# Optimization experiments

Hardware: AMD Instinct MI355X
Metric: run time of the kernel (lower is better)

## Reference

```python
import jax, jax.numpy as jnp
import numpy as np

N = 4_194_304          # number of rays
DAMPING = 0.5          # LM(0.5)
MAX_DELTA = 1000.0     # clamp on LM step
N_ITER = 30            # no_grad warmup iterations
XMIN, XMAX, TAU = -1.0, 1.0, 1.0


def _surface_F(pts, c):
    # implicit parabolic rod: F(p) = x - c*(y^2 + z^2); pts: [N,3]
    return pts[..., 0] - c * (pts[..., 1] ** 2 + pts[..., 2] ** 2)


def _lm_delta(P, V, t, c):
    # Levenberg-Marquardt step for f(t) = F(P + t*V):
    # delta = f * f' / (f'^2 + damping), clamped to [-max_delta, max_delta]
    pts = P + t[:, None] * V                     # [N,3]
    f = _surface_F(pts, c)                       # [N]
    # f'(t) = gradF(pts) . V, gradF = (1, -2c*y, -2c*z)
    fp = V[:, 0] - 2.0 * c * (pts[:, 1] * V[:, 1] + pts[:, 2] * V[:, 2])
    delta = f * fp / (fp * fp + DAMPING)
    return jnp.clip(delta, -MAX_DELTA, MAX_DELTA)


def setup_inputs() -> dict:
    key = jax.random.key(0)
    k1, k2 = jax.random.split(key, 2)
    P = jax.random.normal(k1, (N, 3), jnp.float32) * 2.0
    V = jax.random.normal(k2, (N, 3), jnp.float32)
    V = V / jnp.linalg.norm(V, axis=-1, keepdims=True)
    a, b = 0.3, -0.2
    Rz = jnp.array([[np.cos(a), -np.sin(a), 0.0],
                    [np.sin(a),  np.cos(a), 0.0],
                    [0.0,        0.0,       1.0]], jnp.float32)
    Ry = jnp.array([[np.cos(b), 0.0, np.sin(b)],
                    [0.0,       1.0, 0.0],
                    [-np.sin(b), 0.0, np.cos(b)]], jnp.float32)
    R = Rz @ Ry                                  # rigid rotation [3,3]
    T = jnp.array([0.1, -0.2, 0.05], jnp.float32)
    c = jnp.float32(0.05)
    loss_in = jnp.float32(0.0)
    return {"P": P, "V": V, "R": R, "T": T, "c": c, "loss_in": loss_in}


def reference(P, V, R, T, c, loss_in):
    n = P.shape[0]
    # transform.inverse_points / inverse_vectors: R^T (p - T), R^T v
    P_local = (P - T) @ R                        # [N,3]
    V_local = V @ R                              # [N,3]

    # 30 no-grad LM iterations (torch.no_grad -> stop_gradient on inputs)
    Pl = jax.lax.stop_gradient(P_local)
    Vl = jax.lax.stop_gradient(V_local)
    cs = jax.lax.stop_gradient(c)

    def body(i, t):
        return t - _lm_delta(Pl, Vl, t, cs)

    t0 = jax.lax.fori_loop(0, N_ITER, body, jnp.zeros((n,), jnp.float32))

    # final differentiable LM step
    t = t0 - _lm_delta(P_local, V_local, t0, c)

    points_local = P_local + t[:, None] * V_local
    scale = jnp.mean(jnp.abs(jnp.array([XMIN, XMAX, TAU], jnp.float32)))
    F = _surface_F(points_local, c) / scale
    loss = loss_in + jnp.sum(F ** 2) / n
    return loss
```

## Files before the change

kernel.cpp:

```cpp
#include <hip/hip_runtime.h>


#define LM_ITERS 31
constexpr float DAMPING = 0.5f;

__global__ __launch_bounds__(256) void rod_kernel(
    const float* __restrict__ P, const float* __restrict__ V,
    const float* __restrict__ Rm, const float* __restrict__ Tv,
    const float* __restrict__ c_ptr, double* __restrict__ ws, int n)
{
    const float c  = c_ptr[0];
    const float r00 = Rm[0], r01 = Rm[1], r02 = Rm[2];
    const float r10 = Rm[3], r11 = Rm[4], r12 = Rm[5];
    const float r20 = Rm[6], r21 = Rm[7], r22 = Rm[8];
    const float t0 = Tv[0], t1 = Tv[1], t2 = Tv[2];

    const int tid      = blockIdx.x * blockDim.x + threadIdx.x;
    const int nthreads = gridDim.x * blockDim.x;

    const float4* P4 = (const float4*)P;
    const float4* V4 = (const float4*)V;

    double acc = 0.0;

    float nA[4], f[4], fp[4];
    auto setup4 = [&](const float4& qa, const float4& qb, const float4& qc,
                      const float4& ua, const float4& ub, const float4& uc) {
        const float px[4] = {qa.x, qa.w, qb.z, qc.y};
        const float py[4] = {qa.y, qb.x, qb.w, qc.z};
        const float pz[4] = {qa.z, qb.y, qc.x, qc.w};
        const float wx[4] = {ua.x, ua.w, ub.z, uc.y};
        const float wy[4] = {ua.y, ub.x, ub.w, uc.z};
        const float wz[4] = {ua.z, ub.y, uc.x, uc.w};
        #pragma unroll
        for (int r = 0; r < 4; ++r) {
            const float qx = px[r] - t0, qy = py[r] - t1, qz = pz[r] - t2;
            const float plx = qx * r00 + qy * r10 + qz * r20;
            const float ply = qx * r01 + qy * r11 + qz * r21;
            const float plz = qx * r02 + qy * r12 + qz * r22;
            const float vlx = wx[r] * r00 + wy[r] * r10 + wz[r] * r20;
            const float vly = wx[r] * r01 + wy[r] * r11 + wz[r] * r21;
            const float vlz = wx[r] * r02 + wy[r] * r12 + wz[r] * r22;
            nA[r] = c * (vly * vly + vlz * vlz);
            f[r]  = plx - c * (ply * ply + plz * plz);
            fp[r] = vlx - 2.0f * c * (ply * vly + plz * vlz);
        }
    };

    auto iterate = [&]() {
        #pragma unroll 1
        for (int it = 0; it < LM_ITERS; ++it) {
            #pragma unroll
            for (int r = 0; r < 4; ++r) {
                const float den = fmaf(fp[r], fp[r], DAMPING);
                const float rcp = __builtin_amdgcn_rcpf(den);
                const float d   = (f[r] * fp[r]) * rcp;
                const float tmp = fmaf(nA[r], d, fp[r]);
                f[r]  = fmaf(-d, tmp, f[r]);
                fp[r] = fmaf(nA[r], d, tmp);
            }
        }
    };

    auto accum = [&](int g) {
        #pragma unroll
        for (int r = 0; r < 4; ++r)
            if (4 * g + r < n) acc += (double)f[r] * (double)f[r];
    };

    const int g0 = tid;
    const int g1 = tid + nthreads;
    const int g2 = tid + 2 * nthreads;
    const int g3 = tid + 3 * nthreads;

    float4 a0{}, b0{}, c0{}, u0{}, v0{}, w0{};
    if (4 * g0 < n) {
        a0 = P4[g0 * 3 + 0]; b0 = P4[g0 * 3 + 1]; c0 = P4[g0 * 3 + 2];
        u0 = V4[g0 * 3 + 0]; v0 = V4[g0 * 3 + 1]; w0 = V4[g0 * 3 + 2];
    }
    setup4(a0, b0, c0, u0, v0, w0);

    float4 a1{}, b1{}, c1{}, u1{}, v1{}, w1{};
    if (4 * g1 < n) {
        a1 = P4[g1 * 3 + 0]; b1 = P4[g1 * 3 + 1]; c1 = P4[g1 * 3 + 2];
        u1 = V4[g1 * 3 + 0]; v1 = V4[g1 * 3 + 1]; w1 = V4[g1 * 3 + 2];
    }
    iterate();
    accum(g0);

    setup4(a1, b1, c1, u1, v1, w1);
    float4 a2{}, b2{}, c2{}, u2{}, v2{}, w2{};
    if (4 * g2 < n) {
        a2 = P4[g2 * 3 + 0]; b2 = P4[g2 * 3 + 1]; c2 = P4[g2 * 3 + 2];
        u2 = V4[g2 * 3 + 0]; v2 = V4[g2 * 3 + 1]; w2 = V4[g2 * 3 + 2];
    }
    iterate();
    accum(g1);

    setup4(a2, b2, c2, u2, v2, w2);
    float4 a3{}, b3{}, c3{}, u3{}, v3{}, w3{};
    if (4 * g3 < n) {
        a3 = P4[g3 * 3 + 0]; b3 = P4[g3 * 3 + 1]; c3 = P4[g3 * 3 + 2];
        u3 = V4[g3 * 3 + 0]; v3 = V4[g3 * 3 + 1]; w3 = V4[g3 * 3 + 2];
    }
    iterate();
    accum(g2);

    setup4(a3, b3, c3, u3, v3, w3);
    iterate();
    accum(g3);

    for (int off = 32; off > 0; off >>= 1)
        acc += __shfl_down(acc, off, 64);
    __shared__ double sacc[4];
    const int lane = threadIdx.x & 63, wave = threadIdx.x >> 6;
    if (lane == 0) sacc[wave] = acc;
    __syncthreads();
    if (threadIdx.x == 0) {
        atomicAdd(ws, sacc[0] + sacc[1] + sacc[2] + sacc[3]);
    }
}

__global__ void rod_finalize(const double* __restrict__ ws,
                             const float* __restrict__ loss_in,
                             float* __restrict__ out, double inv_n)
{
    out[0] = (float)(ws[0] * inv_n + (double)loss_in[0]);
}

extern "C" void kernel_launch(void* const* d_in, const int* in_sizes, int n_in,
                              void* d_out, int out_size, void* d_ws, size_t ws_size,
                              hipStream_t stream) {
    const float* P       = (const float*)d_in[0];
    const float* V       = (const float*)d_in[1];
    const float* R       = (const float*)d_in[2];
    const float* T       = (const float*)d_in[3];
    const float* c       = (const float*)d_in[4];
    const float* loss_in = (const float*)d_in[5];

    const int n = in_sizes[0] / 3;

    hipMemsetAsync(d_ws, 0, sizeof(double), stream);

    const int threads = (n + 15) / 16;
    const int block   = 256;
    const int grid    = (threads + block - 1) / block;
    rod_kernel<<<grid, block, 0, stream>>>(P, V, R, T, c, (double*)d_ws, n);
    rod_finalize<<<1, 1, 0, stream>>>((const double*)d_ws, loss_in,
                                      (float*)d_out, 1.0 / (double)n);
}
```

Baseline: 135.6 us.

## Stage ray loads through LDS with global_load_lds, one group of rays per thread

Replaces the four-group-per-thread grid-stride scheme, which prefetched the next group during the LM loop, with one group of four rays per thread and four times as many threads. Each wave loads its contiguous P and V chunk into LDS with global_load_lds direct-to-LDS copies, so the global loads are fully coalesced, then reads the interleaved xyz back per lane. The cost is losing the software overlap of loads with compute and quadrupling the block count and atomics, relying on occupancy instead. A scalar fallback path handles partial tail waves.

```diff
diff --git a/kernel.cpp b/kernel.cpp
--- a/kernel.cpp
+++ b/kernel.cpp
@@ -1,8 +1,12 @@
 #include <hip/hip_runtime.h>
+#include <stdint.h>
 
 
 #define LM_ITERS 31
 constexpr float DAMPING = 0.5f;
+
+typedef __attribute__((address_space(3))) uint32_t lds_u32_t;
+typedef __attribute__((address_space(1))) const uint32_t glob_u32_t;
 
 __global__ __launch_bounds__(256) void rod_kernel(
     const float* __restrict__ P, const float* __restrict__ V,
@@ -15,105 +19,100 @@
     const float r20 = Rm[6], r21 = Rm[7], r22 = Rm[8];
     const float t0 = Tv[0], t1 = Tv[1], t2 = Tv[2];
 
-    const int tid      = blockIdx.x * blockDim.x + threadIdx.x;
-    const int nthreads = gridDim.x * blockDim.x;
+    __shared__ float4 sh[4][192];
 
-    const float4* P4 = (const float4*)P;
-    const float4* V4 = (const float4*)V;
+    const int lane = threadIdx.x & 63;
+    const int wave = threadIdx.x >> 6;
+    const int wave_ray_base = blockIdx.x * 1024 + wave * 256;
+    const int base_ray      = wave_ray_base + 4 * lane;
+
+    float px[4], py[4], pz[4], wx[4], wy[4], wz[4];
+
+    if (wave_ray_base + 256 <= n) {
+        const size_t wq = (size_t)(wave_ray_base >> 2) * 3;
+        const char* gP = (const char*)P + wq * 16;
+        const char* gV = (const char*)V + wq * 16;
+
+        #pragma unroll
+        for (int j = 0; j < 3; ++j) {
+            __builtin_amdgcn_global_load_lds(
+                (glob_u32_t*)(gP + (size_t)(j * 64 + lane) * 16),
+                (lds_u32_t*)&sh[wave][j * 64 + lane], 16, 0, 0);
+        }
+        asm volatile("s_waitcnt vmcnt(0)" ::: "memory");
+        const float4 pa = sh[wave][lane * 3 + 0];
+        const float4 pb = sh[wave][lane * 3 + 1];
+        const float4 pc = sh[wave][lane * 3 + 2];
+        asm volatile("s_waitcnt lgkmcnt(0)" ::: "memory");
+
+        #pragma unroll
+        for (int j = 0; j < 3; ++j) {
+            __builtin_amdgcn_global_load_lds(
+                (glob_u32_t*)(gV + (size_t)(j * 64 + lane) * 16),
+                (lds_u32_t*)&sh[wave][j * 64 + lane], 16, 0, 0);
+        }
+        asm volatile("s_waitcnt vmcnt(0)" ::: "memory");
+        const float4 va = sh[wave][lane * 3 + 0];
+        const float4 vb = sh[wave][lane * 3 + 1];
+        const float4 vc = sh[wave][lane * 3 + 2];
+        asm volatile("s_waitcnt lgkmcnt(0)" ::: "memory");
+
+        px[0] = pa.x; px[1] = pa.w; px[2] = pb.z; px[3] = pc.y;
+        py[0] = pa.y; py[1] = pb.x; py[2] = pb.w; py[3] = pc.z;
+        pz[0] = pa.z; pz[1] = pb.y; pz[2] = pc.x; pz[3] = pc.w;
+        wx[0] = va.x; wx[1] = va.w; wx[2] = vb.z; wx[3] = vc.y;
+        wy[0] = va.y; wy[1] = vb.x; wy[2] = vb.w; wy[3] = vc.z;
+        wz[0] = va.z; wz[1] = vb.y; wz[2] = vc.x; wz[3] = vc.w;
+    } else {
+        #pragma unroll
+        for (int r = 0; r < 4; ++r) {
+            const int ray = base_ray + r;
+            if (ray < n) {
+                px[r] = P[3 * ray + 0]; py[r] = P[3 * ray + 1]; pz[r] = P[3 * ray + 2];
+                wx[r] = V[3 * ray + 0]; wy[r] = V[3 * ray + 1]; wz[r] = V[3 * ray + 2];
+            } else {
+                px[r] = py[r] = pz[r] = 0.0f;
+                wx[r] = wy[r] = wz[r] = 0.0f;
+            }
+        }
+    }
+
+    float nA[4], f[4], fp[4];
+    #pragma unroll
+    for (int r = 0; r < 4; ++r) {
+        const float qx = px[r] - t0, qy = py[r] - t1, qz = pz[r] - t2;
+        const float plx = qx * r00 + qy * r10 + qz * r20;
+        const float ply = qx * r01 + qy * r11 + qz * r21;
+        const float plz = qx * r02 + qy * r12 + qz * r22;
+        const float vlx = wx[r] * r00 + wy[r] * r10 + wz[r] * r20;
+        const float vly = wx[r] * r01 + wy[r] * r11 + wz[r] * r21;
+        const float vlz = wx[r] * r02 + wy[r] * r12 + wz[r] * r22;
+        nA[r] = c * (vly * vly + vlz * vlz);
+        f[r]  = plx - c * (ply * ply + plz * plz);
+        fp[r] = vlx - 2.0f * c * (ply * vly + plz * vlz);
+    }
+
+    #pragma unroll 1
+    for (int it = 0; it < LM_ITERS; ++it) {
+        #pragma unroll
+        for (int r = 0; r < 4; ++r) {
+            const float den = fmaf(fp[r], fp[r], DAMPING);
+            const float rcp = __builtin_amdgcn_rcpf(den);
+            const float d   = (f[r] * fp[r]) * rcp;
+            const float tmp = fmaf(nA[r], d, fp[r]);
+            f[r]  = fmaf(-d, tmp, f[r]);
+            fp[r] = fmaf(nA[r], d, tmp);
+        }
+    }
 
     double acc = 0.0;
-
-    float nA[4], f[4], fp[4];
-    auto setup4 = [&](const float4& qa, const float4& qb, const float4& qc,
-                      const float4& ua, const float4& ub, const float4& uc) {
-        const float px[4] = {qa.x, qa.w, qb.z, qc.y};
-        const float py[4] = {qa.y, qb.x, qb.w, qc.z};
-        const float pz[4] = {qa.z, qb.y, qc.x, qc.w};
-        const float wx[4] = {ua.x, ua.w, ub.z, uc.y};
-        const float wy[4] = {ua.y, ub.x, ub.w, uc.z};
-        const float wz[4] = {ua.z, ub.y, uc.x, uc.w};
-        #pragma unroll
-        for (int r = 0; r < 4; ++r) {
-            const float qx = px[r] - t0, qy = py[r] - t1, qz = pz[r] - t2;
-            const float plx = qx * r00 + qy * r10 + qz * r20;
-            const float ply = qx * r01 + qy * r11 + qz * r21;
-            const float plz = qx * r02 + qy * r12 + qz * r22;
-            const float vlx = wx[r] * r00 + wy[r] * r10 + wz[r] * r20;
-            const float vly = wx[r] * r01 + wy[r] * r11 + wz[r] * r21;
-            const float vlz = wx[r] * r02 + wy[r] * r12 + wz[r] * r22;
-            nA[r] = c * (vly * vly + vlz * vlz);
-            f[r]  = plx - c * (ply * ply + plz * plz);
-            fp[r] = vlx - 2.0f * c * (ply * vly + plz * vlz);
-        }
-    };
-
-    auto iterate = [&]() {
-        #pragma unroll 1
-        for (int it = 0; it < LM_ITERS; ++it) {
-            #pragma unroll
-            for (int r = 0; r < 4; ++r) {
-                const float den = fmaf(fp[r], fp[r], DAMPING);
-                const float rcp = __builtin_amdgcn_rcpf(den);
-                const float d   = (f[r] * fp[r]) * rcp;
-                const float tmp = fmaf(nA[r], d, fp[r]);
-                f[r]  = fmaf(-d, tmp, f[r]);
-                fp[r] = fmaf(nA[r], d, tmp);
-            }
-        }
-    };
-
-    auto accum = [&](int g) {
-        #pragma unroll
-        for (int r = 0; r < 4; ++r)
-            if (4 * g + r < n) acc += (double)f[r] * (double)f[r];
-    };
-
-    const int g0 = tid;
-    const int g1 = tid + nthreads;
-    const int g2 = tid + 2 * nthreads;
-    const int g3 = tid + 3 * nthreads;
-
-    float4 a0{}, b0{}, c0{}, u0{}, v0{}, w0{};
-    if (4 * g0 < n) {
-        a0 = P4[g0 * 3 + 0]; b0 = P4[g0 * 3 + 1]; c0 = P4[g0 * 3 + 2];
-        u0 = V4[g0 * 3 + 0]; v0 = V4[g0 * 3 + 1]; w0 = V4[g0 * 3 + 2];
-    }
-    setup4(a0, b0, c0, u0, v0, w0);
-
-    float4 a1{}, b1{}, c1{}, u1{}, v1{}, w1{};
-    if (4 * g1 < n) {
-        a1 = P4[g1 * 3 + 0]; b1 = P4[g1 * 3 + 1]; c1 = P4[g1 * 3 + 2];
-        u1 = V4[g1 * 3 + 0]; v1 = V4[g1 * 3 + 1]; w1 = V4[g1 * 3 + 2];
-    }
-    iterate();
-    accum(g0);
-
-    setup4(a1, b1, c1, u1, v1, w1);
-    float4 a2{}, b2{}, c2{}, u2{}, v2{}, w2{};
-    if (4 * g2 < n) {
-        a2 = P4[g2 * 3 + 0]; b2 = P4[g2 * 3 + 1]; c2 = P4[g2 * 3 + 2];
-        u2 = V4[g2 * 3 + 0]; v2 = V4[g2 * 3 + 1]; w2 = V4[g2 * 3 + 2];
-    }
-    iterate();
-    accum(g1);
-
-    setup4(a2, b2, c2, u2, v2, w2);
-    float4 a3{}, b3{}, c3{}, u3{}, v3{}, w3{};
-    if (4 * g3 < n) {
-        a3 = P4[g3 * 3 + 0]; b3 = P4[g3 * 3 + 1]; c3 = P4[g3 * 3 + 2];
-        u3 = V4[g3 * 3 + 0]; v3 = V4[g3 * 3 + 1]; w3 = V4[g3 * 3 + 2];
-    }
-    iterate();
-    accum(g2);
-
-    setup4(a3, b3, c3, u3, v3, w3);
-    iterate();
-    accum(g3);
+    #pragma unroll
+    for (int r = 0; r < 4; ++r)
+        if (base_ray + r < n) acc += (double)f[r] * (double)f[r];
 
     for (int off = 32; off > 0; off >>= 1)
         acc += __shfl_down(acc, off, 64);
     __shared__ double sacc[4];
-    const int lane = threadIdx.x & 63, wave = threadIdx.x >> 6;
     if (lane == 0) sacc[wave] = acc;
     __syncthreads();
     if (threadIdx.x == 0) {
@@ -142,7 +141,7 @@
 
     hipMemsetAsync(d_ws, 0, sizeof(double), stream);
 
-    const int threads = (n + 15) / 16;
+    const int threads = (n + 3) / 4;
     const int block   = 256;
     const int grid    = (threads + block - 1) / block;
     rod_kernel<<<grid, block, 0, stream>>>(P, V, R, T, c, (double*)d_ws, n);
```

After: 164.3 us. +21.1%, slower.
